# Optimization experiments

Measured on AMD Instinct MI355X. Metric: run time of the kernel, lower is better.

## Reference

```python
import jax, jax.numpy as jnp
import numpy as np

B, T, C, D = 64, 4096, 51, 64
MASK_PROB = 0.3
LN_EPS = 1e-5


def setup_inputs() -> dict:
    key = jax.random.key(0)
    k0, k1, k2, k3, k4 = jax.random.split(key, 5)
    x = jax.random.normal(k0, (B, T, C), dtype=jnp.float32)
    # xavier_uniform_ then *= 0.5 (as in reset_parameters)
    bound = float(np.sqrt(6.0 / (C + D)))
    W = jax.random.uniform(k1, (C, D), jnp.float32, -bound, bound) * 0.5
    Wm = jax.random.uniform(k2, (C, D), jnp.float32, -bound, bound) * 0.5
    gamma = jnp.ones((D,), jnp.float32)
    beta = jnp.zeros((D,), jnp.float32)
    time_mask = jax.random.bernoulli(k3, MASK_PROB, (B, T))
    sensor_mask = jax.random.bernoulli(k4, MASK_PROB, (B, C))
    return {"x": x, "W": W, "Wm": Wm, "gamma": gamma, "beta": beta,
            "time_mask": time_mask, "sensor_mask": sensor_mask}


def reference(x, W, Wm, gamma, beta, time_mask, sensor_mask):
    # mask[b,t,c] = time_mask[b,t] OR sensor_mask[b,c]
    mask = (time_mask[:, :, None] | sensor_mask[:, None, :]).astype(x.dtype)  # [B,T,C]
    # Fused masked reductions (math-equivalent to the broadcast [B,T,C,D] path)
    xu = jnp.einsum('btc,cd->btd', x * (1.0 - mask), W)   # [B,T,D]
    xm = jnp.einsum('btc,cd->btd', mask, Wm)              # [B,T,D]
    out = xu + xm
    # LayerNorm over last dim
    mu = jnp.mean(out, axis=-1, keepdims=True)
    var = jnp.mean((out - mu) ** 2, axis=-1, keepdims=True)
    out = (out - mu) * jax.lax.rsqrt(var + LN_EPS) * gamma + beta
    return out
```

## Files before the change

kernel.cpp:

```cpp
#include <hip/hip_runtime.h>

#define BB 64
#define TT 4096
#define CC 51
#define DD 64
#define LN_EPS 1e-5f

typedef __attribute__((ext_vector_type(8))) short short8;
typedef __attribute__((ext_vector_type(4))) float f32x4;

union FragU { int i[4]; short8 s; };

#define DPP_QP_1032   0xB1
#define DPP_QP_2301   0x4E
#define DPP_ROW_HMIRR 0x141
#define DPP_ROW_MIRR  0x140

__device__ __forceinline__ float dpp_add(float v, int tag) {
  int t;
  switch (tag) {
    case 0: t = __builtin_amdgcn_update_dpp(0, __float_as_int(v), DPP_QP_1032,   0xF, 0xF, true); break;
    case 1: t = __builtin_amdgcn_update_dpp(0, __float_as_int(v), DPP_QP_2301,   0xF, 0xF, true); break;
    case 2: t = __builtin_amdgcn_update_dpp(0, __float_as_int(v), DPP_ROW_HMIRR, 0xF, 0xF, true); break;
    default: t = __builtin_amdgcn_update_dpp(0, __float_as_int(v), DPP_ROW_MIRR, 0xF, 0xF, true); break;
  }
  return v + __int_as_float(t);
}
__device__ __forceinline__ float allsum16(float v) {
  v = dpp_add(v, 0); v = dpp_add(v, 1); v = dpp_add(v, 2); v = dpp_add(v, 3);
  return v;
}
__device__ __forceinline__ float allsum64(float v) {
  v = allsum16(v);
  v += __shfl_xor(v, 16, 64);
  v += __shfl_xor(v, 32, 64);
  return v;
}

__device__ __forceinline__ int pack_hl(float x) {
  const unsigned u = __float_as_uint(x);
  const unsigned h = u >> 16;
  const float hf = __uint_as_float(u & 0xFFFF0000u);
  const unsigned l = __float_as_uint(x - hf) >> 16;
  return (int)(h | (l << 16));
}

__global__ void ipmask_setup3(const float* __restrict__ Wm,
                              const float* __restrict__ gamma,
                              const float* __restrict__ beta,
                              const int* __restrict__ smask,
                              float* __restrict__ ws) {
  __shared__ float red[8][64];
  const int t = threadIdx.x, L = t & 63, w = t >> 6;
  const int b = blockIdx.x;
  const int c0 = w * 13, c1 = (c0 + 13 < CC) ? c0 + 13 : CC;
  float bs = 0.0f, f = 0.0f;
  for (int c = c0; c < c1; ++c) {
    const float wmv = Wm[c * DD + L];
    const float sf = (float)smask[b * CC + c];
    bs = fmaf(sf, wmv, bs);
    f += wmv;
  }
  red[w * 2][L] = bs;
  red[w * 2 + 1][L] = f;
  __syncthreads();
  if (w == 0) {
    bs = (red[0][L] + red[2][L]) + (red[4][L] + red[6][L]);
    f  = (red[1][L] + red[3][L]) + (red[5][L] + red[7][L]);
    ws[b * 128 + L] = bs;
    const float s1 = allsum64(f);
    const float s2 = allsum64(f * f);
    const float mu = s1 * (1.0f / 64.0f);
    const float vr = fmaf(-mu, mu, s2 * (1.0f / 64.0f));
    const float rs = rsqrtf(vr + LN_EPS);
    ws[b * 128 + 64 + L] = fmaf((f - mu) * rs, gamma[L], beta[L]);
  }
}

__global__ __launch_bounds__(256, 2)
void ipmask_mfma3(const float* __restrict__ x, const float* __restrict__ W,
                  const float* __restrict__ gamma, const float* __restrict__ beta,
                  const int* __restrict__ tmask, const int* __restrict__ smask,
                  const float* __restrict__ ws, float* __restrict__ out) {
  const int t = threadIdx.x, L = t & 63;
  const int q = L >> 4, m16 = L & 15;
  const int gw = (blockIdx.x << 2) + (t >> 6);
  const int b = gw >> 6;
  const int rowBase = (b << 12) + ((gw & 63) << 6);

  const int* smB = smask + b * CC;

  float xf[4][4][4];
#pragma unroll
  for (int mt = 0; mt < 4; ++mt) {
    const float* xr = x + (size_t)(rowBase + mt * 16 + m16) * CC;
#pragma unroll
    for (int ks = 0; ks < 4; ++ks) {
#pragma unroll
      for (int j = 0; j < 4; ++j) {
        const int c = ks * 16 + q * 4 + j;
        xf[mt][ks][j] = (c < CC) ? xr[c] : 0.0f;
      }
    }
  }
  const int tmv = tmask[rowBase + L];

  f32x4 acc[4][4];
#pragma unroll
  for (int nt = 0; nt < 4; ++nt) {
    const float bias_nt = ws[b * 128 + nt * 16 + m16];
#pragma unroll
    for (int mt = 0; mt < 4; ++mt) {
      acc[mt][nt][0] = bias_nt; acc[mt][nt][1] = bias_nt;
      acc[mt][nt][2] = bias_nt; acc[mt][nt][3] = bias_nt;
    }
  }

#pragma unroll
  for (int ks = 0; ks < 4; ++ks) {
    FragU bmu[4], bcu[4];
#pragma unroll
    for (int j = 0; j < 4; ++j) {
      const int c = ks * 16 + q * 4 + j;
      const int smv = (c < CC) ? smB[c] : 1;
#pragma unroll
      for (int nt = 0; nt < 4; ++nt) {
        const int n = nt * 16 + m16;
        float we = 0.0f;
        if (c < CC) we = W[c * DD + n];
        if (smv) we = 0.0f;
        const unsigned u = __float_as_uint(we);
        const unsigned h = u >> 16;
        const float hf = __uint_as_float(u & 0xFFFF0000u);
        const unsigned l = __float_as_uint(we - hf) >> 16;
        bmu[nt].i[j] = (int)(h | (h << 16));
        bcu[nt].i[j] = (int)l;
      }
    }
#pragma unroll
    for (int mt = 0; mt < 4; ++mt) {
      FragU au;
#pragma unroll
      for (int j = 0; j < 4; ++j) au.i[j] = pack_hl(xf[mt][ks][j]);
#pragma unroll
      for (int nt = 0; nt < 4; ++nt) {
        acc[mt][nt] = __builtin_amdgcn_mfma_f32_16x16x32_bf16(au.s, bmu[nt].s, acc[mt][nt], 0, 0, 0);
        acc[mt][nt] = __builtin_amdgcn_mfma_f32_16x16x32_bf16(au.s, bcu[nt].s, acc[mt][nt], 0, 0, 0);
      }
    }
  }

  float g_[4], b_[4], cons_[4];
#pragma unroll
  for (int nt = 0; nt < 4; ++nt) {
    g_[nt] = gamma[nt * 16 + m16];
    b_[nt] = beta[nt * 16 + m16];
    cons_[nt] = ws[b * 128 + 64 + nt * 16 + m16];
  }
#pragma unroll
  for (int mt = 0; mt < 4; ++mt) {
#pragma unroll
    for (int rg = 0; rg < 4; ++rg) {
      float su = 0.0f, sq = 0.0f;
#pragma unroll
      for (int nt = 0; nt < 4; ++nt) {
        const float v = acc[mt][nt][rg];
        su += v;
        sq = fmaf(v, v, sq);
      }
      su = allsum16(su);
      sq = allsum16(sq);
      const float mu = su * (1.0f / 64.0f);
      const float vr = fmaf(-mu, mu, sq * (1.0f / 64.0f));
      const float rs = rsqrtf(vr + LN_EPS);
      const int rloc = mt * 16 + q * 4 + rg;
      const int tm = __shfl(tmv, rloc, 64);
      const size_t obase = (size_t)(rowBase + rloc) * DD;
#pragma unroll
      for (int nt = 0; nt < 4; ++nt) {
        float val = fmaf((acc[mt][nt][rg] - mu) * rs, g_[nt], b_[nt]);
        if (tm) val = cons_[nt];
        __builtin_nontemporal_store(val, &out[obase + nt * 16 + m16]);
      }
    }
  }
}

extern "C" void kernel_launch(void* const* d_in, const int* in_sizes, int n_in,
                              void* d_out, int out_size, void* d_ws, size_t ws_size,
                              hipStream_t stream) {
  const float* x     = (const float*)d_in[0];
  const float* W     = (const float*)d_in[1];
  const float* Wm    = (const float*)d_in[2];
  const float* gamma = (const float*)d_in[3];
  const float* beta  = (const float*)d_in[4];
  const int*   tmask = (const int*)d_in[5];
  const int*   smask = (const int*)d_in[6];
  float* out = (float*)d_out;
  float* ws  = (float*)d_ws;

  ipmask_setup3<<<dim3(BB), dim3(256), 0, stream>>>(Wm, gamma, beta, smask, ws);
  ipmask_mfma3<<<dim3(1024), dim3(256), 0, stream>>>(
      x, W, gamma, beta, tmask, smask, ws, out);
}
```

Baseline: 129.3 us.

## Fuse setup into main MFMA kernel and halve rows per wave

Removes the separate setup kernel: each wave now computes the masked-bias and constant LayerNorm row from Wm and the sensor mask itself, passing values between lanes with shuffles instead of a workspace buffer. Rows per wave drop from 64 to 32, giving 2048 blocks, and launch bounds are raised to 4 blocks per SM. Input x is packed into bf16 hi/lo fragments at load time. This cuts a kernel launch and the dependency between the two kernels, but every wave now redoes the 51-step Wm reduction and the W fragment construction on half as many rows.

Result: slower. 142.6 us (+10.3%).

```diff
diff --git a/kernel.cpp b/kernel.cpp
--- a/kernel.cpp
+++ b/kernel.cpp
@@ -45,72 +45,60 @@
   return (int)(h | (l << 16));
 }
 
-__global__ void ipmask_setup3(const float* __restrict__ Wm,
-                              const float* __restrict__ gamma,
-                              const float* __restrict__ beta,
-                              const int* __restrict__ smask,
-                              float* __restrict__ ws) {
-  __shared__ float red[8][64];
-  const int t = threadIdx.x, L = t & 63, w = t >> 6;
-  const int b = blockIdx.x;
-  const int c0 = w * 13, c1 = (c0 + 13 < CC) ? c0 + 13 : CC;
-  float bs = 0.0f, f = 0.0f;
-  for (int c = c0; c < c1; ++c) {
-    const float wmv = Wm[c * DD + L];
-    const float sf = (float)smask[b * CC + c];
-    bs = fmaf(sf, wmv, bs);
-    f += wmv;
-  }
-  red[w * 2][L] = bs;
-  red[w * 2 + 1][L] = f;
-  __syncthreads();
-  if (w == 0) {
-    bs = (red[0][L] + red[2][L]) + (red[4][L] + red[6][L]);
-    f  = (red[1][L] + red[3][L]) + (red[5][L] + red[7][L]);
-    ws[b * 128 + L] = bs;
-    const float s1 = allsum64(f);
-    const float s2 = allsum64(f * f);
-    const float mu = s1 * (1.0f / 64.0f);
-    const float vr = fmaf(-mu, mu, s2 * (1.0f / 64.0f));
-    const float rs = rsqrtf(vr + LN_EPS);
-    ws[b * 128 + 64 + L] = fmaf((f - mu) * rs, gamma[L], beta[L]);
-  }
-}
-
-__global__ __launch_bounds__(256, 2)
-void ipmask_mfma3(const float* __restrict__ x, const float* __restrict__ W,
-                  const float* __restrict__ gamma, const float* __restrict__ beta,
-                  const int* __restrict__ tmask, const int* __restrict__ smask,
-                  const float* __restrict__ ws, float* __restrict__ out) {
+__global__ __launch_bounds__(256, 4)
+void ipmask_fused7(const float* __restrict__ x, const float* __restrict__ W,
+                   const float* __restrict__ Wm, const float* __restrict__ gamma,
+                   const float* __restrict__ beta, const int* __restrict__ tmask,
+                   const int* __restrict__ smask, float* __restrict__ out) {
   const int t = threadIdx.x, L = t & 63;
   const int q = L >> 4, m16 = L & 15;
   const int gw = (blockIdx.x << 2) + (t >> 6);
-  const int b = gw >> 6;
-  const int rowBase = (b << 12) + ((gw & 63) << 6);
+  const int b  = gw >> 7;
+  const int rowBase = (b << 12) + ((gw & 127) << 5);
 
   const int* smB = smask + b * CC;
 
-  float xf[4][4][4];
+  FragU au[2][4];
 #pragma unroll
-  for (int mt = 0; mt < 4; ++mt) {
+  for (int mt = 0; mt < 2; ++mt) {
     const float* xr = x + (size_t)(rowBase + mt * 16 + m16) * CC;
 #pragma unroll
     for (int ks = 0; ks < 4; ++ks) {
 #pragma unroll
       for (int j = 0; j < 4; ++j) {
         const int c = ks * 16 + q * 4 + j;
-        xf[mt][ks][j] = (c < CC) ? xr[c] : 0.0f;
+        float xv = 0.0f;
+        if (c < CC) xv = xr[c];
+        au[mt][ks].i[j] = pack_hl(xv);
       }
     }
   }
-  const int tmv = tmask[rowBase + L];
+  const int tmv = tmask[rowBase + (L & 31)];
 
-  f32x4 acc[4][4];
+  float bs = 0.0f, f = 0.0f;
+#pragma unroll
+  for (int c = 0; c < CC; ++c) {
+    const float wmv = Wm[c * DD + L];
+    const float sf = (float)smB[c];
+    bs = fmaf(sf, wmv, bs);
+    f += wmv;
+  }
+  float constL;
+  {
+    const float s1 = allsum64(f);
+    const float s2 = allsum64(f * f);
+    const float mu = s1 * (1.0f / 64.0f);
+    const float vr = fmaf(-mu, mu, s2 * (1.0f / 64.0f));
+    const float rs = rsqrtf(vr + LN_EPS);
+    constL = (f - mu) * rs;
+  }
+
+  f32x4 acc[2][4];
 #pragma unroll
   for (int nt = 0; nt < 4; ++nt) {
-    const float bias_nt = ws[b * 128 + nt * 16 + m16];
+    const float bias_nt = __shfl(bs, nt * 16 + m16, 64);
 #pragma unroll
-    for (int mt = 0; mt < 4; ++mt) {
+    for (int mt = 0; mt < 2; ++mt) {
       acc[mt][nt][0] = bias_nt; acc[mt][nt][1] = bias_nt;
       acc[mt][nt][2] = bias_nt; acc[mt][nt][3] = bias_nt;
     }
@@ -138,14 +126,11 @@
       }
     }
 #pragma unroll
-    for (int mt = 0; mt < 4; ++mt) {
-      FragU au;
-#pragma unroll
-      for (int j = 0; j < 4; ++j) au.i[j] = pack_hl(xf[mt][ks][j]);
+    for (int mt = 0; mt < 2; ++mt) {
 #pragma unroll
       for (int nt = 0; nt < 4; ++nt) {
-        acc[mt][nt] = __builtin_amdgcn_mfma_f32_16x16x32_bf16(au.s, bmu[nt].s, acc[mt][nt], 0, 0, 0);
-        acc[mt][nt] = __builtin_amdgcn_mfma_f32_16x16x32_bf16(au.s, bcu[nt].s, acc[mt][nt], 0, 0, 0);
+        acc[mt][nt] = __builtin_amdgcn_mfma_f32_16x16x32_bf16(au[mt][ks].s, bmu[nt].s, acc[mt][nt], 0, 0, 0);
+        acc[mt][nt] = __builtin_amdgcn_mfma_f32_16x16x32_bf16(au[mt][ks].s, bcu[nt].s, acc[mt][nt], 0, 0, 0);
       }
     }
   }
@@ -153,12 +138,13 @@
   float g_[4], b_[4], cons_[4];
 #pragma unroll
   for (int nt = 0; nt < 4; ++nt) {
-    g_[nt] = gamma[nt * 16 + m16];
-    b_[nt] = beta[nt * 16 + m16];
-    cons_[nt] = ws[b * 128 + 64 + nt * 16 + m16];
+    const int n = nt * 16 + m16;
+    g_[nt] = gamma[n];
+    b_[nt] = beta[n];
+    cons_[nt] = fmaf(__shfl(constL, n, 64), g_[nt], b_[nt]);
   }
 #pragma unroll
-  for (int mt = 0; mt < 4; ++mt) {
+  for (int mt = 0; mt < 2; ++mt) {
 #pragma unroll
     for (int rg = 0; rg < 4; ++rg) {
       float su = 0.0f, sq = 0.0f;
@@ -197,9 +183,7 @@
   const int*   tmask = (const int*)d_in[5];
   const int*   smask = (const int*)d_in[6];
   float* out = (float*)d_out;
-  float* ws  = (float*)d_ws;
 
-  ipmask_setup3<<<dim3(BB), dim3(256), 0, stream>>>(Wm, gamma, beta, smask, ws);
-  ipmask_mfma3<<<dim3(1024), dim3(256), 0, stream>>>(
-      x, W, gamma, beta, tmask, smask, ws, out);
+  ipmask_fused7<<<dim3(2048), dim3(256), 0, stream>>>(
+      x, W, Wm, gamma, beta, tmask, smask, out);
 }
```
